# Kernel optimization log

Hardware: AMD Instinct MI355X
Metric: run time of the kernel (lower is better)

## Reference

```python
import jax, jax.numpy as jnp
from jax import lax
import numpy as np

VOCAB, EMB, HID = 32000, 512, 512
START, STOP = 1, 2
B, T = 32, 32


def setup_inputs() -> dict:
    key = jax.random.key(0)
    ks = jax.random.split(key, 9)
    s = 0.02
    return {
        "x": jax.random.normal(ks[0], (B, HID), jnp.float32),
        "labels": jax.random.randint(ks[1], (B, T), 0, VOCAB),
        "coin": jax.random.randint(ks[2], (B, T), 0, 2).astype(bool),
        "emb": jax.random.normal(ks[3], (VOCAB, EMB), jnp.float32) * s,
        "Wi": jax.random.normal(ks[4], (EMB, 4 * HID), jnp.float32) * s,
        "Wh": jax.random.normal(ks[5], (HID, 4 * HID), jnp.float32) * s,
        "b": jnp.zeros((4 * HID,), jnp.float32),
        "Wo": jax.random.normal(ks[6], (HID, VOCAB), jnp.float32) * s,
        "bo": jnp.zeros((VOCAB,), jnp.float32),
    }


def reference(x, labels, coin, emb, Wi, Wh, b, Wo, bo):
    Bsz, Tlen = labels.shape

    def cell(inp, hn, cn):
        # PyTorch LSTMCell gate order: i, f, g, o
        gates = inp @ Wi + hn @ Wh + b  # [B, 4H]
        i_, f_, g_, o_ = jnp.split(gates, 4, axis=-1)
        cn = jax.nn.sigmoid(f_) * cn + jax.nn.sigmoid(i_) * jnp.tanh(g_)
        hn = jax.nn.sigmoid(o_) * jnp.tanh(cn)
        out = hn @ Wo + bo  # [B, V] logits
        return out, hn, cn

    inp0 = jnp.broadcast_to(emb[START], (Bsz, emb.shape[1]))
    hn0 = x                       # init_states: hidden <- image feature
    cn0 = jnp.zeros_like(x)
    loss0 = jnp.zeros((), jnp.float32)

    def step(carry, t_in):
        inp, hn, cn, loss = carry
        label_t, coin_t = t_in    # [B], [B]
        out, hn, cn = cell(inp, hn, cn)
        logp = jax.nn.log_softmax(out, axis=-1)
        ce = -jnp.take_along_axis(logp, label_t[:, None], axis=1)[:, 0]
        loss = loss + ce.sum()
        pred = jnp.argmax(out, axis=-1)  # scheduled sampling
        next_tok = jnp.where(coin_t, pred, label_t)
        return (emb[next_tok], hn, cn, loss), None

    (inp, hn, cn, loss), _ = lax.scan(step, (inp0, hn0, cn0, loss0), (labels.T, coin.T))

    # final STOP step
    out, hn, cn = cell(inp, hn, cn)
    logp = jax.nn.log_softmax(out, axis=-1)
    loss = loss + (-logp[:, STOP]).sum()
    return loss / Bsz
```

## Files before the change

### kernel.cpp

```cpp
#include <hip/hip_runtime.h>
#include <math.h>

#define VOCABSZ 32000
#define EMBD 512
#define HIDD 512
#define BSZ 32
#define TLEN 32
#define G4 2048
#define NGRP 1000
#define NLB 250
#define PSTRIDE 8192
#define SW 256.0f
#define SH 16.0f
#define INV_SWH (1.0f / (SW * SH))

using bf16x8 = __attribute__((ext_vector_type(8))) short;
using f32x16 = __attribute__((ext_vector_type(16))) float;
typedef long long i64;

__device__ __forceinline__ float sigmoidf_(float x) { return 1.f / (1.f + expf(-x)); }
__device__ __forceinline__ unsigned short f2bf(float f) {
    unsigned u = __float_as_uint(f);
    return (unsigned short)((u + 0x7fffu + ((u >> 16) & 1u)) >> 16);
}
__device__ __forceinline__ unsigned char f2e4m3(float f) {
    unsigned u = __float_as_uint(f);
    unsigned s = (u >> 24) & 0x80u;
    int e = (int)((u >> 23) & 0xffu);
    unsigned m = u & 0x7fffffu;
    int ee = e - 120;
    if (ee >= 16) return (unsigned char)(s | 0x7E);
    if (ee <= 0) return (unsigned char)s;
    unsigned r = m + 0x7FFFFu + ((m >> 20) & 1u);
    if (r & 0x800000u) { ee += 1; r = 0; if (ee >= 16) return (unsigned char)(s | 0x7E); }
    unsigned mant = (r >> 20) & 7u;
    if (ee == 15 && mant == 7u) return (unsigned char)(s | 0x7E);
    return (unsigned char)(s | (unsigned)(ee << 3) | mant);
}

__global__ __launch_bounds__(256) void init7_kernel(
    const float* __restrict__ x, const void* __restrict__ coin,
    float* __restrict__ cst, unsigned short* __restrict__ hbf,
    unsigned char* __restrict__ hf8,
    float* __restrict__ ce_acc, int* __restrict__ flag) {
    __shared__ int s_f;
    int tid = threadIdx.x;
    int i = blockIdx.x * 256 + tid;
    if (blockIdx.x == 0) {
        if (tid == 0) s_f = 0;
        __syncthreads();
        if (((const unsigned int*)coin)[tid] > 1u) s_f = 1;
        __syncthreads();
        if (tid == 0) *flag = s_f;
        if (tid < 32) ce_acc[tid] = 0.f;
    }
    float v = x[i];
    cst[i] = 0.f;
    hbf[i] = f2bf(v);
    hf8[i] = f2e4m3(v * SH);
}

__global__ __launch_bounds__(256) void emb_prep_kernel(
    const float* __restrict__ emb, unsigned short* __restrict__ embbf) {
    size_t i8 = ((size_t)blockIdx.x * 256 + threadIdx.x) * 8;
    float4 a = *(const float4*)&emb[i8];
    float4 b = *(const float4*)&emb[i8 + 4];
    bf16x8 v;
    v[0] = (short)f2bf(a.x); v[1] = (short)f2bf(a.y);
    v[2] = (short)f2bf(a.z); v[3] = (short)f2bf(a.w);
    v[4] = (short)f2bf(b.x); v[5] = (short)f2bf(b.y);
    v[6] = (short)f2bf(b.z); v[7] = (short)f2bf(b.w);
    *(bf16x8*)&embbf[i8] = v;
}

__global__ __launch_bounds__(256) void wot8_prep_kernel(
    const float* __restrict__ Wo, i64* __restrict__ wot8) {
    __shared__ unsigned char s[512 * 32];
    int g = blockIdx.x;
    int tid = threadIdx.x;
    int col = tid & 31;
    int k0 = tid >> 5;
    for (int kk = k0; kk < 512; kk += 8)
        s[kk * 32 + col] = f2e4m3(Wo[(size_t)kk * VOCABSZ + g * 32 + col] * SW);
    __syncthreads();
    for (int f = tid; f < 2048; f += 256) {
        int kt = f >> 6, lane = f & 63;
        int kb = kt * 16 + ((lane >> 5) << 3);
        int c = lane & 31;
        union { unsigned char b[8]; i64 v; } u;
        #pragma unroll
        for (int j = 0; j < 8; ++j) u.b[j] = s[(kb + j) * 32 + c];
        wot8[(size_t)g * 2048 + (kt >> 1) * 128 + lane * 2 + (kt & 1)] = u.v;
    }
}

__global__ __launch_bounds__(256) void wcell_prep_kernel(
    const float* __restrict__ Wi, const float* __restrict__ Wh,
    unsigned short* __restrict__ wcell) {
    __shared__ unsigned short s[512 * 32];
    int cb = blockIdx.x >> 1;
    int half = blockIdx.x & 1;
    const float* Wsrc = half ? Wh : Wi;
    int tid = threadIdx.x;
    int lc = tid & 31;
    int gcol = (lc >> 3) * 512 + cb * 8 + (lc & 7);
    int k0 = tid >> 5;
    for (int kl = k0; kl < 512; kl += 8)
        s[kl * 32 + lc] = f2bf(Wsrc[(size_t)kl * G4 + gcol]);
    __syncthreads();
    bf16x8* out8 = (bf16x8*)wcell;
    for (int f = tid; f < 2048; f += 256) {
        int ktl = f >> 6, lane = f & 63;
        int kb = ktl * 16 + ((lane >> 5) << 3);
        int c = lane & 31;
        bf16x8 v;
        #pragma unroll
        for (int j = 0; j < 8; ++j) v[j] = (short)s[(kb + j) * 32 + c];
        out8[((size_t)cb * 64 + half * 32 + ktl) * 64 + lane] = v;
    }
}

__global__ __launch_bounds__(1024) void cell_mfma4_kernel(
    const float* __restrict__ emb, const unsigned short* __restrict__ embbf,
    const int* __restrict__ labels,
    const void* __restrict__ coin, const int* __restrict__ flag,
    const unsigned short* __restrict__ wcell, const float* __restrict__ bias,
    float* __restrict__ cst, unsigned short* __restrict__ hbf,
    unsigned char* __restrict__ hf8,
    const float* __restrict__ part, float* __restrict__ ce_acc, int t) {
    __shared__ float sg[16][32][32];
    __shared__ float st[32][33];
    __shared__ int s_tok[32];
    int tid = threadIdx.x;
    int cb = blockIdx.x;
    int lane = tid & 63, wv = tid >> 6;

    if (t == 0) {
        if (tid < 32) s_tok[tid] = 1;
    } else {
        int row = tid >> 5, slot = tid & 31;
        int tm1 = t - 1;
        float m = -3.0e38f; int mi = 0;
        for (int ib = slot; ib < NLB; ib += 32) {
            int e = row * 256 + ib;
            float pm = part[e];
            int pi = __float_as_int(part[2 * PSTRIDE + e]);
            if (pm > m || (pm == m && pi < mi)) { m = pm; mi = pi; }
        }
        #pragma unroll
        for (int d = 1; d < 32; d <<= 1) {
            float om = __shfl_xor(m, d);
            int omi = __shfl_xor(mi, d);
            if (om > m || (om == m && omi < mi)) { m = om; mi = omi; }
        }
        if (slot == 0) {
            int lab = labels[row * TLEN + tm1];
            int cn = (*flag) ? (int)((const unsigned char*)coin)[row * TLEN + tm1]
                             : ((const int*)coin)[row * TLEN + tm1];
            s_tok[row] = cn ? mi : lab;
        }
        if (cb == 0) {
            float M = -3.0e38f, S = 0.f, L = -INFINITY;
            for (int ib = slot; ib < NLB; ib += 32) {
                int e = row * 256 + ib;
                float pm = part[e], ps = part[PSTRIDE + e];
                float nM = fmaxf(M, pm);
                S = S * expf(M - nM) + ps * expf(pm - nM);
                M = nM;
                L = fmaxf(L, part[3 * PSTRIDE + e]);
            }
            #pragma unroll
            for (int d = 1; d < 32; d <<= 1) {
                float oM = __shfl_xor(M, d), oS = __shfl_xor(S, d);
                float nM = fmaxf(M, oM);
                S = S * expf(M - nM) + oS * expf(oM - nM);
                M = nM;
                L = fmaxf(L, __shfl_xor(L, d));
            }
            if (slot == 0) ce_acc[row] += (M + logf(S)) - L;
        }
    }
    __syncthreads();

    int r = lane & 31;
    int ksub = (lane >> 5) << 3;
    const bf16x8* wp = (const bf16x8*)wcell + ((size_t)cb * 64 + wv * 4) * 64 + lane;

    f32x16 acc = {};
    if (wv < 8) {
        int tok = s_tok[r];
        if (embbf) {
            const unsigned short* eb = embbf + (size_t)tok * EMBD;
            #pragma unroll
            for (int i = 0; i < 4; ++i) {
                int k = (wv * 4 + i) * 16 + ksub;
                bf16x8 a = *(const bf16x8*)&eb[k];
                acc = __builtin_amdgcn_mfma_f32_32x32x16_bf16(a, wp[i * 64], acc, 0, 0, 0);
            }
        } else {
            const float* ebase = emb + (size_t)tok * EMBD;
            #pragma unroll
            for (int i = 0; i < 4; ++i) {
                int k = (wv * 4 + i) * 16 + ksub;
                float4 e0 = *(const float4*)(ebase + k);
                float4 e1 = *(const float4*)(ebase + k + 4);
                bf16x8 a;
                a[0] = (short)f2bf(e0.x); a[1] = (short)f2bf(e0.y);
                a[2] = (short)f2bf(e0.z); a[3] = (short)f2bf(e0.w);
                a[4] = (short)f2bf(e1.x); a[5] = (short)f2bf(e1.y);
                a[6] = (short)f2bf(e1.z); a[7] = (short)f2bf(e1.w);
                acc = __builtin_amdgcn_mfma_f32_32x32x16_bf16(a, wp[i * 64], acc, 0, 0, 0);
            }
        }
    } else {
        #pragma unroll
        for (int i = 0; i < 4; ++i) {
            int k = (wv * 4 + i) * 16 + ksub - 512;
            bf16x8 a = *(const bf16x8*)&hbf[r * HIDD + k];
            acc = __builtin_amdgcn_mfma_f32_32x32x16_bf16(a, wp[i * 64], acc, 0, 0, 0);
        }
    }

    int half = lane >> 5;
    #pragma unroll
    for (int reg = 0; reg < 16; ++reg) {
        int row = (reg & 3) + 8 * (reg >> 2) + 4 * half;
        sg[wv][row][lane & 31] = acc[reg];
    }
    __syncthreads();

    {
        int row = tid >> 5, lc = tid & 31;
        float s = 0.f;
        #pragma unroll
        for (int w = 0; w < 16; ++w) s += sg[w][row][lc];
        st[row][lc] = s;
    }
    __syncthreads();

    if (tid < 256) {
        int rr = tid >> 3, jj = tid & 7;
        int jh = cb * 8 + jj;
        float i_ = bias[jh]        + st[rr][jj];
        float f_ = bias[jh + 512]  + st[rr][jj + 8];
        float g_ = bias[jh + 1024] + st[rr][jj + 16];
        float o_ = bias[jh + 1536] + st[rr][jj + 24];
        int idx = rr * HIDD + jh;
        float ci = cst[idx];
        float cn = sigmoidf_(f_) * ci + sigmoidf_(i_) * tanhf(g_);
        float hn = sigmoidf_(o_) * tanhf(cn);
        cst[idx] = cn;
        hbf[idx] = f2bf(hn);
        hf8[idx] = f2e4m3(hn * SH);
    }
}

__global__ __launch_bounds__(512, 4) void logits_fp8b_kernel(
    const i64* __restrict__ wot8, const unsigned char* __restrict__ h_f8,
    const float* __restrict__ bo, const int* __restrict__ labels,
    float* __restrict__ part, int t) {
    __shared__ __align__(16) i64 s_h[2048];
    __shared__ float sacc[4][64][17];
    __shared__ int s_lab[32];
    __shared__ float s_pm[4][32], s_ps[4][32], s_pl[4][32], s_pst[4][32];
    __shared__ int s_pi[4][32];
    int tid = threadIdx.x;
    int lane = tid & 63, wv = tid >> 6;
    int p = wv & 3, kh = wv >> 2;

    for (int f = tid; f < 2048; f += 512) {
        int kt = f >> 6, ln = f & 63;
        int row = ln & 31, kb = kt * 16 + ((ln >> 5) << 3);
        s_h[(kt >> 1) * 128 + ln * 2 + (kt & 1)] = *(const i64*)&h_f8[row * 512 + kb];
    }
    if (tid < 32) s_lab[tid] = labels[tid * TLEN + t];
    __syncthreads();

    int g = blockIdx.x * 4 + p;
    const ulonglong2* wp16 = (const ulonglong2*)(wot8 + (size_t)g * 2048) + lane;
    const ulonglong2* sh16 = (const ulonglong2*)s_h + lane;

    f32x16 acc0 = {}, acc1 = {};
    #pragma unroll
    for (int i = 0; i < 8; ++i) {
        int ktp = kh * 8 + i;
        ulonglong2 ah = sh16[ktp * 64];
        ulonglong2 wq = wp16[ktp * 64];
        acc0 = __builtin_amdgcn_mfma_f32_32x32x16_fp8_fp8(
            (i64)ah.x, (i64)wq.x, acc0, 0, 0, 0);
        acc1 = __builtin_amdgcn_mfma_f32_32x32x16_fp8_fp8(
            (i64)ah.y, (i64)wq.y, acc1, 0, 0, 0);
    }

    if (kh == 1) {
        #pragma unroll
        for (int reg = 0; reg < 16; ++reg)
            sacc[p][lane][reg] = acc0[reg] + acc1[reg];
    }
    __syncthreads();

    if (kh == 0) {
        int half = lane >> 5;
        int colw = lane & 31;
        int col = g * 32 + colw;
        float bq = bo[col];
        #pragma unroll
        for (int reg = 0; reg < 16; ++reg) {
            int row = (reg & 3) + 8 * (reg >> 2) + 4 * half;
            float v = (acc0[reg] + acc1[reg] + sacc[p][lane][reg]) * INV_SWH + bq;
            float m = v; int mi = col;
            #pragma unroll
            for (int d = 1; d < 32; d <<= 1) {
                float om = __shfl_xor(m, d);
                int omi = __shfl_xor(mi, d);
                if (om > m || (om == m && omi < mi)) { m = om; mi = omi; }
            }
            float e = expf(v - m), ssum = e;
            #pragma unroll
            for (int d = 1; d < 32; d <<= 1) ssum += __shfl_xor(ssum, d);
            int labc = s_lab[row];
            float lv = __shfl(v, (labc & 31) + (half << 5));
            if ((labc >> 5) != g) lv = -INFINITY;
            float sv = __shfl(v, 2 + (half << 5));
            if (g != 0) sv = -INFINITY;
            if (colw == 0) {
                s_pm[p][row] = m; s_ps[p][row] = ssum; s_pi[p][row] = mi;
                s_pl[p][row] = lv; s_pst[p][row] = sv;
            }
        }
    }
    __syncthreads();

    if (tid < 32) {
        int row = tid;
        float M = s_pm[0][row], S = s_ps[0][row];
        int MI = s_pi[0][row];
        float L = s_pl[0][row], ST = s_pst[0][row];
        #pragma unroll
        for (int w = 1; w < 4; ++w) {
            float pm = s_pm[w][row], ps = s_ps[w][row];
            int pi = s_pi[w][row];
            float nM = fmaxf(M, pm);
            S = S * expf(M - nM) + ps * expf(pm - nM);
            if (pm > M || (pm == M && pi < MI)) MI = pi;
            M = nM;
            L = fmaxf(L, s_pl[w][row]);
            ST = fmaxf(ST, s_pst[w][row]);
        }
        int e0 = row * 256 + blockIdx.x;
        part[e0] = M;
        part[PSTRIDE + e0] = S;
        part[2 * PSTRIDE + e0] = __int_as_float(MI);
        part[3 * PSTRIDE + e0] = L;
        part[4 * PSTRIDE + e0] = ST;
    }
}

__global__ __launch_bounds__(256) void finalize5_kernel(
    const float* __restrict__ part, const float* __restrict__ ce_acc,
    float* __restrict__ out) {
    __shared__ float s_ce[32];
    int tid = threadIdx.x;
    int row = tid >> 3, slot = tid & 7;
    float M = -3.0e38f, S = 0.f, ST = -INFINITY;
    for (int ib = slot; ib < NLB; ib += 8) {
        int e = row * 256 + ib;
        float pm = part[e], ps = part[PSTRIDE + e];
        float nM = fmaxf(M, pm);
        S = S * expf(M - nM) + ps * expf(pm - nM);
        M = nM;
        ST = fmaxf(ST, part[4 * PSTRIDE + e]);
    }
    #pragma unroll
    for (int d = 1; d < 8; d <<= 1) {
        float oM = __shfl_xor(M, d), oS = __shfl_xor(S, d);
        float nM = fmaxf(M, oM);
        S = S * expf(M - nM) + oS * expf(oM - nM);
        M = nM;
        ST = fmaxf(ST, __shfl_xor(ST, d));
    }
    if (slot == 0) s_ce[row] = ce_acc[row] + (M + logf(S)) - ST;
    __syncthreads();
    if (tid == 0) {
        float tot = 0.f;
        for (int r = 0; r < 32; ++r) tot += s_ce[r];
        *out = tot / 32.f;
    }
}

extern "C" void kernel_launch(void* const* d_in, const int* in_sizes, int n_in,
                              void* d_out, int out_size, void* d_ws, size_t ws_size,
                              hipStream_t stream) {
    const float* x      = (const float*)d_in[0];
    const int*   labels = (const int*)  d_in[1];
    const void*  coin   =               d_in[2];
    const float* emb    = (const float*)d_in[3];
    const float* Wi     = (const float*)d_in[4];
    const float* Wh     = (const float*)d_in[5];
    const float* b      = (const float*)d_in[6];
    const float* Wo     = (const float*)d_in[7];
    const float* bo     = (const float*)d_in[8];

    float* ws     = (float*)d_ws;
    float* cst    = ws;
    unsigned short* h_bf = (unsigned short*)(ws + 16384);
    unsigned char*  h_f8 = (unsigned char*)(ws + 24576);
    float* part   = ws + 28672;
    float* ce_acc = ws + 69632;
    int*   flag   = (int*)(ws + 69664);
    unsigned short* wcell = (unsigned short*)(ws + 69696);
    i64*   wot8   = (i64*)(ws + 69696 + 1048576);
    unsigned short* embbf = (unsigned short*)(ws + 69696 + 1048576 + 4096000);
    float* outp   = (float*)d_out;

    size_t need_emb = (size_t)(69696 + 1048576 + 4096000 + 8192000) * 4;
    const unsigned short* embbf_use = (ws_size >= need_emb) ? embbf : (const unsigned short*)0;

    wot8_prep_kernel<<<NGRP, 256, 0, stream>>>(Wo, wot8);
    wcell_prep_kernel<<<128, 256, 0, stream>>>(Wi, Wh, wcell);
    if (embbf_use)
        emb_prep_kernel<<<VOCABSZ * EMBD / 2048, 256, 0, stream>>>(emb, embbf);
    init7_kernel<<<64, 256, 0, stream>>>(x, coin, cst, h_bf, h_f8, ce_acc, flag);

    for (int t = 0; t < 33; ++t) {
        int tt = (t < 32) ? t : 0;
        cell_mfma4_kernel<<<64, 1024, 0, stream>>>(emb, embbf_use, labels, coin,
                                                   flag, wcell, b, cst, h_bf,
                                                   h_f8, part, ce_acc, t);
        logits_fp8b_kernel<<<NLB, 512, 0, stream>>>(wot8, h_f8, bo, labels,
                                                    part, tt);
    }
    finalize5_kernel<<<1, 256, 0, stream>>>(part, ce_acc, outp);
}
```

Baseline: 1.072 ms.

## Split logits K-loop four ways and double block count to 500

The logits kernel now gives each block 2 column groups instead of 4, with 4 waves splitting the K dimension per group instead of 2, and launches 500 blocks instead of 250. Each wave also loads all four of its weight fragments up front before the MFMA chain. The aim is more parallelism across CUs and more memory-level parallelism when streaming the FP8 output weights. In exchange the partial-result buffer doubles, so the cell and finalize kernels must reduce over twice as many partials, and more shared-memory accumulator traffic is needed.

```diff
diff --git a/kernel.cpp b/kernel.cpp
--- a/kernel.cpp
+++ b/kernel.cpp
@@ -8,8 +8,9 @@
 #define TLEN 32
 #define G4 2048
 #define NGRP 1000
-#define NLB 250
-#define PSTRIDE 8192
+#define NLB 500
+#define SSTRIDE 512
+#define PSTRIDE 16384
 #define SW 256.0f
 #define SH 16.0f
 #define INV_SWH (1.0f / (SW * SH))
@@ -142,7 +143,7 @@
         int tm1 = t - 1;
         float m = -3.0e38f; int mi = 0;
         for (int ib = slot; ib < NLB; ib += 32) {
-            int e = row * 256 + ib;
+            int e = row * SSTRIDE + ib;
             float pm = part[e];
             int pi = __float_as_int(part[2 * PSTRIDE + e]);
             if (pm > m || (pm == m && pi < mi)) { m = pm; mi = pi; }
@@ -162,7 +163,7 @@
         if (cb == 0) {
             float M = -3.0e38f, S = 0.f, L = -INFINITY;
             for (int ib = slot; ib < NLB; ib += 32) {
-                int e = row * 256 + ib;
+                int e = row * SSTRIDE + ib;
                 float pm = part[e], ps = part[PSTRIDE + e];
                 float nM = fmaxf(M, pm);
                 S = S * expf(M - nM) + ps * expf(pm - nM);
@@ -255,18 +256,18 @@
     }
 }
 
-__global__ __launch_bounds__(512, 4) void logits_fp8b_kernel(
+__global__ __launch_bounds__(512, 4) void logits_fp8c_kernel(
     const i64* __restrict__ wot8, const unsigned char* __restrict__ h_f8,
     const float* __restrict__ bo, const int* __restrict__ labels,
     float* __restrict__ part, int t) {
     __shared__ __align__(16) i64 s_h[2048];
-    __shared__ float sacc[4][64][17];
+    __shared__ float sacc[2][3][64][17];
     __shared__ int s_lab[32];
-    __shared__ float s_pm[4][32], s_ps[4][32], s_pl[4][32], s_pst[4][32];
-    __shared__ int s_pi[4][32];
+    __shared__ float s_pm[2][32], s_ps[2][32], s_pl[2][32], s_pst[2][32];
+    __shared__ int s_pi[2][32];
     int tid = threadIdx.x;
     int lane = tid & 63, wv = tid >> 6;
-    int p = wv & 3, kh = wv >> 2;
+    int p = wv & 1, kq = wv >> 1;
 
     for (int f = tid; f < 2048; f += 512) {
         int kt = f >> 6, ln = f & 63;
@@ -276,30 +277,32 @@
     if (tid < 32) s_lab[tid] = labels[tid * TLEN + t];
     __syncthreads();
 
-    int g = blockIdx.x * 4 + p;
+    int g = blockIdx.x * 2 + p;
     const ulonglong2* wp16 = (const ulonglong2*)(wot8 + (size_t)g * 2048) + lane;
     const ulonglong2* sh16 = (const ulonglong2*)s_h + lane;
 
+    ulonglong2 wq[4];
+    #pragma unroll
+    for (int i = 0; i < 4; ++i) wq[i] = wp16[(kq * 4 + i) * 64];
+
     f32x16 acc0 = {}, acc1 = {};
     #pragma unroll
-    for (int i = 0; i < 8; ++i) {
-        int ktp = kh * 8 + i;
-        ulonglong2 ah = sh16[ktp * 64];
-        ulonglong2 wq = wp16[ktp * 64];
+    for (int i = 0; i < 4; ++i) {
+        ulonglong2 ah = sh16[(kq * 4 + i) * 64];
         acc0 = __builtin_amdgcn_mfma_f32_32x32x16_fp8_fp8(
-            (i64)ah.x, (i64)wq.x, acc0, 0, 0, 0);
+            (i64)ah.x, (i64)wq[i].x, acc0, 0, 0, 0);
         acc1 = __builtin_amdgcn_mfma_f32_32x32x16_fp8_fp8(
-            (i64)ah.y, (i64)wq.y, acc1, 0, 0, 0);
-    }
-
-    if (kh == 1) {
+            (i64)ah.y, (i64)wq[i].y, acc1, 0, 0, 0);
+    }
+
+    if (kq > 0) {
         #pragma unroll
         for (int reg = 0; reg < 16; ++reg)
-            sacc[p][lane][reg] = acc0[reg] + acc1[reg];
-    }
-    __syncthreads();
-
-    if (kh == 0) {
+            sacc[p][kq - 1][lane][reg] = acc0[reg] + acc1[reg];
+    }
+    __syncthreads();
+
+    if (kq == 0) {
         int half = lane >> 5;
         int colw = lane & 31;
         int col = g * 32 + colw;
@@ -307,7 +310,9 @@
         #pragma unroll
         for (int reg = 0; reg < 16; ++reg) {
             int row = (reg & 3) + 8 * (reg >> 2) + 4 * half;
-            float v = (acc0[reg] + acc1[reg] + sacc[p][lane][reg]) * INV_SWH + bq;
+            float v = (acc0[reg] + acc1[reg] + sacc[p][0][lane][reg]
+                       + sacc[p][1][lane][reg] + sacc[p][2][lane][reg])
+                      * INV_SWH + bq;
             float m = v; int mi = col;
             #pragma unroll
             for (int d = 1; d < 32; d <<= 1) {
@@ -336,18 +341,17 @@
         float M = s_pm[0][row], S = s_ps[0][row];
         int MI = s_pi[0][row];
         float L = s_pl[0][row], ST = s_pst[0][row];
-        #pragma unroll
-        for (int w = 1; w < 4; ++w) {
-            float pm = s_pm[w][row], ps = s_ps[w][row];
-            int pi = s_pi[w][row];
+        {
+            float pm = s_pm[1][row], ps = s_ps[1][row];
+            int pi = s_pi[1][row];
             float nM = fmaxf(M, pm);
             S = S * expf(M - nM) + ps * expf(pm - nM);
             if (pm > M || (pm == M && pi < MI)) MI = pi;
             M = nM;
-            L = fmaxf(L, s_pl[w][row]);
-            ST = fmaxf(ST, s_pst[w][row]);
-        }
-        int e0 = row * 256 + blockIdx.x;
+            L = fmaxf(L, s_pl[1][row]);
+            ST = fmaxf(ST, s_pst[1][row]);
+        }
+        int e0 = row * SSTRIDE + blockIdx.x;
         part[e0] = M;
         part[PSTRIDE + e0] = S;
         part[2 * PSTRIDE + e0] = __int_as_float(MI);
@@ -364,7 +368,7 @@
     int row = tid >> 3, slot = tid & 7;
     float M = -3.0e38f, S = 0.f, ST = -INFINITY;
     for (int ib = slot; ib < NLB; ib += 8) {
-        int e = row * 256 + ib;
+        int e = row * SSTRIDE + ib;
         float pm = part[e], ps = part[PSTRIDE + e];
         float nM = fmaxf(M, pm);
         S = S * expf(M - nM) + ps * expf(pm - nM);
@@ -406,14 +410,14 @@
     unsigned short* h_bf = (unsigned short*)(ws + 16384);
     unsigned char*  h_f8 = (unsigned char*)(ws + 24576);
     float* part   = ws + 28672;
-    float* ce_acc = ws + 69632;
-    int*   flag   = (int*)(ws + 69664);
-    unsigned short* wcell = (unsigned short*)(ws + 69696);
-    i64*   wot8   = (i64*)(ws + 69696 + 1048576);
-    unsigned short* embbf = (unsigned short*)(ws + 69696 + 1048576 + 4096000);
+    float* ce_acc = ws + 110592;
+    int*   flag   = (int*)(ws + 110624);
+    unsigned short* wcell = (unsigned short*)(ws + 110656);
+    i64*   wot8   = (i64*)(ws + 110656 + 1048576);
+    unsigned short* embbf = (unsigned short*)(ws + 110656 + 1048576 + 4096000);
     float* outp   = (float*)d_out;
 
-    size_t need_emb = (size_t)(69696 + 1048576 + 4096000 + 8192000) * 4;
+    size_t need_emb = (size_t)(110656 + 1048576 + 4096000 + 8192000) * 4;
     const unsigned short* embbf_use = (ws_size >= need_emb) ? embbf : (const unsigned short*)0;
 
     wot8_prep_kernel<<<NGRP, 256, 0, stream>>>(Wo, wot8);
@@ -427,7 +431,7 @@
         cell_mfma4_kernel<<<64, 1024, 0, stream>>>(emb, embbf_use, labels, coin,
                                                    flag, wcell, b, cst, h_bf,
                                                    h_f8, part, ce_acc, t);
-        logits_fp8b_kernel<<<NLB, 512, 0, stream>>>(wot8, h_f8, bo, labels,
+        logits_fp8c_kernel<<<NLB, 512, 0, stream>>>(wot8, h_f8, bo, labels,
                                                     part, tt);
     }
     finalize5_kernel<<<1, 256, 0, stream>>>(part, ce_acc, outp);
```

After: 1.281 ms. 1.19x slower.
